# Optimization experiments

Hardware: AMD Instinct MI355X
Metric: run time of the kernel (lower is better)

The kernel has to match this reference:

```python
import jax, jax.numpy as jnp
import numpy as np
import math

NLAT, NLON, LMAX, MMAX = 128, 256, 50, 50
K = 3  # three_nn

# ---- precompute: Clenshaw-Curtis quadrature (torch_harmonics 'equiangular') ----
def _cc_nodes_weights(n):
    Nn = n - 1
    theta = np.pi * np.arange(n) / Nn
    v = np.zeros(n)
    for k in range(1, Nn // 2 + 1):
        b = 1.0 if 2 * k == Nn else 2.0
        v += b * np.cos(2 * k * theta) / (4 * k * k - 1)
    w = (2.0 / Nn) * (1.0 - v)
    w[0] *= 0.5
    w[-1] *= 0.5
    return np.cos(theta), w

# ---- precompute: orthonormal associated Legendre P_l^m(cos theta), csphase ----
def _legpoly(lmax, mmax, cost):
    sint = np.sqrt(np.clip(1.0 - cost ** 2, 0.0, None))
    p = np.zeros((mmax, lmax, cost.shape[0]))
    pmm = np.full(cost.shape[0], np.sqrt(1.0 / (4.0 * np.pi)))
    for m in range(mmax):
        if m > 0:
            pmm = -pmm * np.sqrt((2.0 * m + 1.0) / (2.0 * m)) * sint
        p[m, m] = pmm
        if m + 1 < lmax:
            p[m, m + 1] = np.sqrt(2.0 * m + 3.0) * cost * pmm
        for l in range(m + 2, lmax):
            a = np.sqrt((4.0 * l * l - 1.0) / (l * l - m * m))
            b = np.sqrt(((2.0 * l + 1.0) * (l - 1 + m) * (l - 1 - m)) / ((2.0 * l - 3.0) * (l * l - m * m)))
            p[m, l] = a * cost * p[m, l - 1] - b * p[m, l - 2]
    return p

_cost, _w = _cc_nodes_weights(NLAT)
_PCTW = jnp.asarray((_legpoly(LMAX, MMAX, _cost) * _w[None, None, :]).astype(np.float32))  # (mmax,lmax,nlat)

_gx, _gy = np.meshgrid(np.arange(NLAT), np.arange(-NLAT, NLAT), indexing='ij')
_GRID = jnp.asarray((np.stack([_gx.ravel(), _gy.ravel()], -1) / NLAT * np.pi).astype(np.float32))  # (M,2)

_RECTW = jnp.asarray(np.exp(-(LMAX - np.arange(1, LMAX + 1)) ** 2 / (2.0 * LMAX ** 2)).astype(np.float32))  # (lmax,)


def to_spherical(coords):
    # coords: (B,N,3) -> r:(B,N), sph:(B,N,2) = [arccos(x/r), azimuth in [0,2pi)]
    sq = coords ** 2
    pn = jnp.sqrt(jnp.flip(jnp.cumsum(jnp.flip(sq, -1), -1), -1))  # pn[...,i] = ||coords[...,i:]||
    r = pn[..., 0]
    phi = jnp.arccos(coords[..., :-2] / pn[..., :-2])
    a = jnp.arccos(coords[..., -2] / pn[..., -2])
    phi_final = a + (2.0 * math.pi - 2.0 * a) * (coords[..., -1] < 0)
    return r, jnp.concatenate([phi, phi_final[..., None]], axis=-1)


def interp_to_grid(coords):
    # spherical transform + 3-NN (squared dists) + distance-weighted interpolation onto the lat/lon grid
    r, sph = to_spherical(coords)
    sph = sph.at[..., 1].add(-math.pi)
    # brute-force pairwise squared distances grid(M,2) vs sph(B,N,2): (B,M,N)
    d2 = (jnp.sum(_GRID ** 2, -1)[None, :, None] + jnp.sum(sph ** 2, -1)[:, None, :]
          - 2.0 * jnp.einsum('md,bnd->bmn', _GRID, sph))
    _, idx = jax.lax.top_k(-jax.lax.stop_gradient(d2), K)  # (B,M,K), ascending distance
    sel = jax.vmap(lambda s, i: s[i])(sph, idx)            # (B,M,K,2)
    fsel = jax.vmap(lambda f, i: f[i])(r, idx)             # (B,M,K)
    dk = jnp.sum((_GRID[None, :, None, :] - sel) ** 2, -1)  # recompute selected sq-dists (differentiable)
    w = dk / jnp.sum(dk, -1, keepdims=True)                # weights = dist / sum(dist), as in source
    return jnp.sum(fsel * w, -1).reshape(-1, NLAT, NLON)


def sht_real(x):
    # RealSHT (equiangular, ortho): rfft(norm='forward')*2pi, then Legendre*quadrature einsum; real part only
    xf = jnp.fft.rfft(x, axis=-1)[..., :MMAX] * (2.0 * math.pi / NLON)
    return jnp.einsum('bkm,mlk->blm', jnp.real(xf).astype(jnp.float32), _PCTW)  # (B,lmax,mmax)


def setup_inputs() -> dict:
    key = jax.random.key(0)
    k1, k2 = jax.random.split(key)
    pred = jax.random.normal(k1, (2, 2048, 3), dtype=jnp.float32)
    target = jax.random.normal(k2, (2, 2048, 3), dtype=jnp.float32)
    return {"pred": pred, "target": target}


def reference(pred, target):
    pc = sht_real(interp_to_grid(pred))
    tc = sht_real(interp_to_grid(target))
    return jnp.mean(jnp.sum((pc - tc) ** 2 * _RECTW[None, :, None], axis=(1, 2)))
```

## Files before the change

### kernel.cpp

```cpp
#include <hip/hip_runtime.h>
#include <math.h>

#define PI_D 3.14159265358979323846
#define PIF  3.14159265358979323846f
#define NLAT 128
#define NLON 256
#define LMAX 50
#define MMAX 50
#define NPTS 2048
#define NBT 16
#define NBA 32
#define NBIN (NBT * NBA)
#define WBIN 0.19634954084936207f
#define INVW 5.092958178940651f
#define BIG 1e30f

__device__ __forceinline__ void insert3(float d, float& k0, float& k1, float& k2) {
    float n1 = __builtin_amdgcn_fmed3f(d, k0, k1);
    float n2 = __builtin_amdgcn_fmed3f(d, k1, k2);
    k0 = fminf(d, k0);
    k1 = n1;
    k2 = n2;
}

__global__ __launch_bounds__(256) void fused_main(
    const float* __restrict__ pred, const float* __restrict__ tgt,
    float* __restrict__ pctwT, float* __restrict__ fre, float* __restrict__ out) {

    __shared__ float2 s_btl[NPTS];
    __shared__ float  s_br[NPTS];
    __shared__ int    s_cnt[NBIN];
    __shared__ int    s_off[NBIN + 1];
    __shared__ float  ctab[NLON];
    __shared__ float  row[NLON];
    __shared__ float  part[200];

    int bid = blockIdx.x;
    int t = threadIdx.x;

    if (bid >= 512) {
        int k = bid - 512;
        if (k == 0 && t == 0) out[0] = 0.0f;
        if (t < MMAX) {
            int m = t;
            double theta = PI_D * (double)k / 127.0;
            double cost = cos(theta);
            double sint = sqrt(fmax(1.0 - cost * cost, 0.0));
            double c2 = cos(2.0 * theta);
            double two_c2 = 2.0 * c2;
            double cp = 1.0, cc = c2, v = 0.0;
            for (int tt = 1; tt <= 63; ++tt) {
                v += 2.0 * cc / (double)(4 * tt * tt - 1);
                double cn = two_c2 * cc - cp;
                cp = cc;
                cc = cn;
            }
            double w = (2.0 / 127.0) * (1.0 - v);
            if (k == 0 || k == 127) w *= 0.5;

            double pmm = sqrt(1.0 / (4.0 * PI_D));
            for (int i = 1; i <= m; ++i)
                pmm = -pmm * sqrt((2.0 * (double)i + 1.0) / (2.0 * (double)i)) * sint;

            float* o = pctwT + (size_t)k * MMAX + m;
            for (int l = 0; l < m; ++l) o[(size_t)l * NLAT * MMAX] = 0.0f;
            o[(size_t)m * NLAT * MMAX] = (float)(pmm * w);
            double plm2 = pmm, plm1 = 0.0;
            if (m + 1 < LMAX) {
                plm1 = sqrt(2.0 * (double)m + 3.0) * cost * pmm;
                o[(size_t)(m + 1) * NLAT * MMAX] = (float)(plm1 * w);
            }
            for (int l = m + 2; l < LMAX; ++l) {
                double ll = (double)l;
                double denom = ll * ll - (double)(m * m);
                double a = sqrt((4.0 * ll * ll - 1.0) / denom);
                double b = sqrt(((2.0 * ll + 1.0) * (double)(l - 1 + m) * (double)(l - 1 - m)) /
                                ((2.0 * ll - 3.0) * denom));
                double p = a * cost * plm1 - b * plm2;
                o[(size_t)l * NLAT * MMAX] = (float)(p * w);
                plm2 = plm1;
                plm1 = p;
            }
        }
        return;
    }

    int f = bid >> 7;
    int lat = bid & 127;
    const float* src = ((f < 2) ? pred : tgt) + (size_t)(f & 1) * NPTS * 3;

    s_cnt[t] = 0;
    s_cnt[t + 256] = 0;
    ctab[t] = (float)cos(2.0 * PI_D * (double)t / (double)NLON);
    __syncthreads();

    float pth[8], paz[8], pr[8];
    int pbin[8];
#pragma unroll
    for (int i = 0; i < 8; ++i) {
        int n = t + 256 * i;
        float x = src[3 * n], y = src[3 * n + 1], z = src[3 * n + 2];
        float s1 = z * z;
        float s2 = s1 + y * y;
        float s3 = s2 + x * x;
        float r = sqrtf(s3);
        float rho = sqrtf(s2);
        float th = acosf(x / r);
        float a = acosf(y / rho);
        float az = (z < 0.0f) ? (a + (2.0f * PIF - 2.0f * a)) : a;
        az -= PIF;
        int bt = min(max((int)(th * INVW), 0), NBT - 1);
        int ba = min(max((int)((az + PIF) * INVW), 0), NBA - 1);
        int b = bt * NBA + ba;
        pth[i] = th; paz[i] = az; pr[i] = r; pbin[i] = b;
        atomicAdd(&s_cnt[b], 1);
    }
    __syncthreads();

    if (t == 0) s_off[NBIN] = NPTS;
    if (t < 64) {
        int base = t * 8;
        int loc[8];
        int run = 0;
#pragma unroll
        for (int i = 0; i < 8; ++i) { loc[i] = run; run += s_cnt[base + i]; }
        int x = run;
#pragma unroll
        for (int d = 1; d < 64; d <<= 1) {
            int y = __shfl_up(x, d);
            if (t >= d) x += y;
        }
        int ex = x - run;
#pragma unroll
        for (int i = 0; i < 8; ++i) s_off[base + i] = ex + loc[i];
    }
    __syncthreads();
    s_cnt[t] = s_off[t];
    s_cnt[t + 256] = s_off[t + 256];
    __syncthreads();
#pragma unroll
    for (int i = 0; i < 8; ++i) {
        int pos = atomicAdd(&s_cnt[pbin[i]], 1);
        s_btl[pos] = make_float2(pth[i], paz[i]);
        s_br[pos] = pr[i];
    }
    __syncthreads();

    int j = t;
    float gt = (float)((double)lat * PI_D / 128.0);
    float gl = (float)(((double)j - 128.0) * PI_D / 128.0);
    float glp = gl + PIF;
    int bt0 = lat >> 3;
    int ba0 = j >> 3;

    float k0 = BIG, k1 = BIG, k2 = BIG;
    bool done = false;
    int Rfin = 31;
    for (int R = 0; R <= 31; ++R) {
        if (__all(done)) break;
        if (!done) {
            int btl = bt0 - R, bth = bt0 + R;
            int lo = max(btl, 0), hi = min(bth, NBT - 1);
            int bal = max(ba0 - R, 0), bah = min(ba0 + R, NBA - 1);
            for (int bt = lo; bt <= hi; ++bt) {
                if (bt == btl || bt == bth) {
                    int i0 = s_off[bt * NBA + bal];
                    int i1 = s_off[bt * NBA + bah + 1];
                    for (int i = i0; i < i1; ++i) {
                        float2 tl = s_btl[i];
                        float dt = gt - tl.x, dl = gl - tl.y;
                        float d = fmaf(dt, dt, dl * dl);
                        insert3(d, k0, k1, k2);
                    }
                } else {
                    if (ba0 - R >= 0) {
                        int b = bt * NBA + ba0 - R;
                        for (int i = s_off[b]; i < s_off[b + 1]; ++i) {
                            float2 tl = s_btl[i];
                            float dt = gt - tl.x, dl = gl - tl.y;
                            float d = fmaf(dt, dt, dl * dl);
                            insert3(d, k0, k1, k2);
                        }
                    }
                    if (ba0 + R <= NBA - 1) {
                        int b = bt * NBA + ba0 + R;
                        for (int i = s_off[b]; i < s_off[b + 1]; ++i) {
                            float2 tl = s_btl[i];
                            float dt = gt - tl.x, dl = gl - tl.y;
                            float d = fmaf(dt, dt, dl * dl);
                            insert3(d, k0, k1, k2);
                        }
                    }
                }
            }
            float safe = BIG;
            if (bt0 - R > 0)       safe = fminf(safe, gt - (float)(bt0 - R) * WBIN);
            if (bt0 + R < NBT - 1) safe = fminf(safe, (float)(bt0 + R + 1) * WBIN - gt);
            if (ba0 - R > 0)       safe = fminf(safe, glp - (float)(ba0 - R) * WBIN);
            if (ba0 + R < NBA - 1) safe = fminf(safe, (float)(ba0 + R + 1) * WBIN - glp);
            if (k2 <= safe * safe) { done = true; Rfin = R; }
        }
    }

    float r0 = 0.0f, r1 = 0.0f, r2 = 0.0f;
    bool f0 = false, f1 = false, f2 = false;
    {
        int lo = max(bt0 - Rfin, 0), hi = min(bt0 + Rfin, NBT - 1);
        int bal = max(ba0 - Rfin, 0), bah = min(ba0 + Rfin, NBA - 1);
        for (int bt = lo; bt <= hi; ++bt) {
            int i0 = s_off[bt * NBA + bal];
            int i1 = s_off[bt * NBA + bah + 1];
            for (int i = i0; i < i1; ++i) {
                float2 tl = s_btl[i];
                float dt = gt - tl.x, dl = gl - tl.y;
                float d = fmaf(dt, dt, dl * dl);
                if (d == k0 && !f0)      { r0 = s_br[i]; f0 = true; }
                else if (d == k1 && !f1) { r1 = s_br[i]; f1 = true; }
                else if (d == k2 && !f2) { r2 = s_br[i]; f2 = true; }
            }
        }
    }
    float s = k0 + k1 + k2;
    row[j] = (k0 * r0 + k1 * r1 + k2 * r2) / s;
    __syncthreads();

    if (t < 200) {
        int mm = t >> 2, q = t & 3;
        int bs = q * 64;
        float acc = 0.0f;
        int p = (bs * mm) & (NLON - 1);
        for (int i = 0; i < 64; ++i) {
            acc += row[bs + i] * ctab[p];
            p = (p + mm) & (NLON - 1);
        }
        part[t] = acc;
    }
    __syncthreads();
    if (t < MMAX) {
        const float* pp = part + t * 4;
        fre[(f * NLAT + lat) * MMAX + t] =
            ((pp[0] + pp[1]) + (pp[2] + pp[3])) * (float)(2.0 * PI_D / (double)NLON);
    }
}

__global__ __launch_bounds__(256) void contract_loss(const float* __restrict__ fre,
                                                     const float* __restrict__ pctwT,
                                                     float* __restrict__ out) {
    int b = blockIdx.x / LMAX;
    int l = blockIdx.x % LMAX;
    int mm = threadIdx.x & 63;
    int kq = threadIdx.x >> 6;
    __shared__ float sp[4][64], st_[4][64];
    float pc = 0.0f, tc = 0.0f;
    if (mm < MMAX) {
        const float* pw = pctwT + ((size_t)l * NLAT + kq * 32) * MMAX + mm;
        const float* fp = fre + ((size_t)b * NLAT + kq * 32) * MMAX + mm;
        const float* ft = fre + ((size_t)(2 + b) * NLAT + kq * 32) * MMAX + mm;
#pragma unroll 8
        for (int k = 0; k < 32; ++k) {
            float w = pw[k * MMAX];
            pc += fp[k * MMAX] * w;
            tc += ft[k * MMAX] * w;
        }
    }
    sp[kq][mm] = pc;
    st_[kq][mm] = tc;
    __syncthreads();
    if (threadIdx.x < 64) {
        int m2 = threadIdx.x;
        float pcs = (sp[0][m2] + sp[1][m2]) + (sp[2][m2] + sp[3][m2]);
        float tcs = (st_[0][m2] + st_[1][m2]) + (st_[2][m2] + st_[3][m2]);
        float diff = pcs - tcs;
        double dl_ = (double)(49 - l);
        float rw = (float)exp(-(dl_ * dl_) / 5000.0);
        float contrib = (m2 < MMAX) ? diff * diff * rw * 0.5f : 0.0f;
        for (int off = 32; off > 0; off >>= 1) contrib += __shfl_down(contrib, off);
        if (m2 == 0) atomicAdd(out, contrib);
    }
}

extern "C" void kernel_launch(void* const* d_in, const int* in_sizes, int n_in,
                              void* d_out, int out_size, void* d_ws, size_t ws_size,
                              hipStream_t stream) {
    const float* pred = (const float*)d_in[0];
    const float* tgt = (const float*)d_in[1];
    float* ws = (float*)d_ws;

    float* pctwT = ws;
    float* fre   = ws + 320000;
    float* out = (float*)d_out;

    fused_main<<<640, 256, 0, stream>>>(pred, tgt, pctwT, fre, out);
    contract_loss<<<2 * LMAX, 256, 0, stream>>>(fre, pctwT, out);
}
```

Baseline: 92.43 us.

## Pack point index into distance low bits to drop kNN re-scan pass

The squared distance's low 11 mantissa bits now hold the point index, so the top-3 search yields indices directly. This removes the second pass that re-scanned every bin to find the radii matching k0/k1/k2. The first ring (R=0..1, a 3x3 bin block) is also handled in one unrolled sweep with a single termination check. The cost is a truncated distance key, which can change tie-breaking and neighbor order when distances differ only in those low bits.

```diff
diff --git a/kernel.cpp b/kernel.cpp
--- a/kernel.cpp
+++ b/kernel.cpp
@@ -14,13 +14,20 @@
 #define WBIN 0.19634954084936207f
 #define INVW 5.092958178940651f
 #define BIG 1e30f
-
-__device__ __forceinline__ void insert3(float d, float& k0, float& k1, float& k2) {
-    float n1 = __builtin_amdgcn_fmed3f(d, k0, k1);
-    float n2 = __builtin_amdgcn_fmed3f(d, k1, k2);
-    k0 = fminf(d, k0);
+#define KMASK 0xFFFFF800u
+
+__device__ __forceinline__ void insert3(float kf, float& k0, float& k1, float& k2) {
+    float n1 = __builtin_amdgcn_fmed3f(kf, k0, k1);
+    float n2 = __builtin_amdgcn_fmed3f(kf, k1, k2);
+    k0 = fminf(kf, k0);
     k1 = n1;
     k2 = n2;
+}
+
+__device__ __forceinline__ float mkkey(float gt, float gl, float2 tl, int idx) {
+    float dt = gt - tl.x, dl = gl - tl.y;
+    float d = fmaf(dt, dt, dl * dl);
+    return __uint_as_float((__float_as_uint(d) & KMASK) | (unsigned)idx);
 }
 
 __global__ __launch_bounds__(256) void fused_main(
@@ -154,9 +161,39 @@
     int ba0 = j >> 3;
 
     float k0 = BIG, k1 = BIG, k2 = BIG;
-    bool done = false;
-    int Rfin = 31;
-    for (int R = 0; R <= 31; ++R) {
+
+    {
+        int rtl = max(bt0 - 1, 0), rth = min(bt0 + 1, NBT - 1);
+        int bal = max(ba0 - 1, 0), bah = min(ba0 + 1, NBA - 1);
+        for (int bt = rtl; bt <= rth; ++bt) {
+            int i = s_off[bt * NBA + bal];
+            int i1 = s_off[bt * NBA + bah + 1];
+            for (; i + 4 <= i1; i += 4) {
+                float2 a0 = s_btl[i];
+                float2 a1 = s_btl[i + 1];
+                float2 a2 = s_btl[i + 2];
+                float2 a3 = s_btl[i + 3];
+                insert3(mkkey(gt, gl, a0, i), k0, k1, k2);
+                insert3(mkkey(gt, gl, a1, i + 1), k0, k1, k2);
+                insert3(mkkey(gt, gl, a2, i + 2), k0, k1, k2);
+                insert3(mkkey(gt, gl, a3, i + 3), k0, k1, k2);
+            }
+            for (; i < i1; ++i)
+                insert3(mkkey(gt, gl, s_btl[i], i), k0, k1, k2);
+        }
+    }
+
+    bool done;
+    {
+        float safe = BIG;
+        if (bt0 - 1 > 0)       safe = fminf(safe, gt - (float)(bt0 - 1) * WBIN);
+        if (bt0 + 1 < NBT - 1) safe = fminf(safe, (float)(bt0 + 2) * WBIN - gt);
+        if (ba0 - 1 > 0)       safe = fminf(safe, glp - (float)(ba0 - 1) * WBIN);
+        if (ba0 + 1 < NBA - 1) safe = fminf(safe, (float)(ba0 + 2) * WBIN - glp);
+        done = (k2 <= safe * safe);
+    }
+
+    for (int R = 2; R <= 31; ++R) {
         if (__all(done)) break;
         if (!done) {
             int btl = bt0 - R, bth = bt0 + R;
@@ -166,30 +203,18 @@
                 if (bt == btl || bt == bth) {
                     int i0 = s_off[bt * NBA + bal];
                     int i1 = s_off[bt * NBA + bah + 1];
-                    for (int i = i0; i < i1; ++i) {
-                        float2 tl = s_btl[i];
-                        float dt = gt - tl.x, dl = gl - tl.y;
-                        float d = fmaf(dt, dt, dl * dl);
-                        insert3(d, k0, k1, k2);
-                    }
+                    for (int i = i0; i < i1; ++i)
+                        insert3(mkkey(gt, gl, s_btl[i], i), k0, k1, k2);
                 } else {
                     if (ba0 - R >= 0) {
                         int b = bt * NBA + ba0 - R;
-                        for (int i = s_off[b]; i < s_off[b + 1]; ++i) {
-                            float2 tl = s_btl[i];
-                            float dt = gt - tl.x, dl = gl - tl.y;
-                            float d = fmaf(dt, dt, dl * dl);
-                            insert3(d, k0, k1, k2);
-                        }
+                        for (int i = s_off[b]; i < s_off[b + 1]; ++i)
+                            insert3(mkkey(gt, gl, s_btl[i], i), k0, k1, k2);
                     }
                     if (ba0 + R <= NBA - 1) {
                         int b = bt * NBA + ba0 + R;
-                        for (int i = s_off[b]; i < s_off[b + 1]; ++i) {
-                            float2 tl = s_btl[i];
-                            float dt = gt - tl.x, dl = gl - tl.y;
-                            float d = fmaf(dt, dt, dl * dl);
-                            insert3(d, k0, k1, k2);
-                        }
+                        for (int i = s_off[b]; i < s_off[b + 1]; ++i)
+                            insert3(mkkey(gt, gl, s_btl[i], i), k0, k1, k2);
                     }
                 }
             }
@@ -198,30 +223,26 @@
             if (bt0 + R < NBT - 1) safe = fminf(safe, (float)(bt0 + R + 1) * WBIN - gt);
             if (ba0 - R > 0)       safe = fminf(safe, glp - (float)(ba0 - R) * WBIN);
             if (ba0 + R < NBA - 1) safe = fminf(safe, (float)(ba0 + R + 1) * WBIN - glp);
-            if (k2 <= safe * safe) { done = true; Rfin = R; }
-        }
-    }
-
-    float r0 = 0.0f, r1 = 0.0f, r2 = 0.0f;
-    bool f0 = false, f1 = false, f2 = false;
+            if (k2 <= safe * safe) done = true;
+        }
+    }
+
     {
-        int lo = max(bt0 - Rfin, 0), hi = min(bt0 + Rfin, NBT - 1);
-        int bal = max(ba0 - Rfin, 0), bah = min(ba0 + Rfin, NBA - 1);
-        for (int bt = lo; bt <= hi; ++bt) {
-            int i0 = s_off[bt * NBA + bal];
-            int i1 = s_off[bt * NBA + bah + 1];
-            for (int i = i0; i < i1; ++i) {
-                float2 tl = s_btl[i];
-                float dt = gt - tl.x, dl = gl - tl.y;
-                float d = fmaf(dt, dt, dl * dl);
-                if (d == k0 && !f0)      { r0 = s_br[i]; f0 = true; }
-                else if (d == k1 && !f1) { r1 = s_br[i]; f1 = true; }
-                else if (d == k2 && !f2) { r2 = s_br[i]; f2 = true; }
-            }
-        }
-    }
-    float s = k0 + k1 + k2;
-    row[j] = (k0 * r0 + k1 * r1 + k2 * r2) / s;
+        int i0 = __float_as_uint(k0) & 0x7FF;
+        int i1 = __float_as_uint(k1) & 0x7FF;
+        int i2 = __float_as_uint(k2) & 0x7FF;
+        float2 p0 = s_btl[i0];
+        float2 p1 = s_btl[i1];
+        float2 p2 = s_btl[i2];
+        float dt0 = gt - p0.x, dl0 = gl - p0.y;
+        float dt1 = gt - p1.x, dl1 = gl - p1.y;
+        float dt2 = gt - p2.x, dl2 = gl - p2.y;
+        float d0 = fmaf(dt0, dt0, dl0 * dl0);
+        float d1 = fmaf(dt1, dt1, dl1 * dl1);
+        float d2 = fmaf(dt2, dt2, dl2 * dl2);
+        float s = d0 + d1 + d2;
+        row[j] = (d0 * s_br[i0] + d1 * s_br[i1] + d2 * s_br[i2]) / s;
+    }
     __syncthreads();
 
     if (t < 200) {
```

Result: faster. 86.30 us (-6.6%).
